# Performance work log

Measured on AMD Instinct MI355X. Metric: run time of the kernel, lower is better.

The kernel has to match this reference:

```python
import jax, jax.numpy as jnp
import numpy as np

N_A = 50000; N_B = 50000          # nodes per type
FD = 8; BINS = 32; EMB = 16       # discrete features, bins, per-feature embed dim
HID = 64; ZD = 32                 # hidden_dim, embed_dim
E = 800000                        # edges per relation (avg degree 16)


def setup_inputs() -> dict:
    key = jax.random.key(0)
    ks = iter(jax.random.split(key, 64))
    def nrm(shape, s=0.05):
        return jax.random.normal(next(ks), shape, jnp.float32) * s
    def ri(shape, hi):
        return jax.random.randint(next(ks), shape, 0, hi, dtype=jnp.int32)
    inp = {
        'x_A': ri((N_A, FD), BINS),
        'x_B': ri((N_B, FD), BINS),
        'ei_ab': ri((2, E), N_A),   # src in A, dst in B (N_A == N_B)
        'ei_ba': ri((2, E), N_B),
        'ei_aa': ri((2, E), N_A),
        # per-feature embedding tables [FD, BINS, EMB]
        'emb_A': nrm((FD, BINS, EMB)), 'emb_B': nrm((FD, BINS, EMB)),
        # pre_lin per node type (in = FD*EMB)
        'pre_W_A': nrm((FD * EMB, HID)), 'pre_b_A': nrm((HID,)),
        'pre_W_B': nrm((FD * EMB, HID)), 'pre_b_B': nrm((HID,)),
        # SAGEConv per relation: lin_l (on aggregated msgs, with bias), lin_r (root, no bias)
        'sage_l_W_ab': nrm((HID, HID)), 'sage_l_b_ab': nrm((HID,)), 'sage_r_W_ab': nrm((HID, HID)),
        'sage_l_W_ba': nrm((HID, HID)), 'sage_l_b_ba': nrm((HID,)), 'sage_r_W_ba': nrm((HID, HID)),
        'sage_l_W_aa': nrm((HID, HID)), 'sage_l_b_aa': nrm((HID,)), 'sage_r_W_aa': nrm((HID, HID)),
        # lin_proj per node type
        'proj_W_A': nrm((HID, ZD)), 'proj_b_A': nrm((ZD,)),
        'proj_W_B': nrm((HID, ZD)), 'proj_b_B': nrm((ZD,)),
        # feature heads per node type -> FD*BINS logits
        'head_W_A': nrm((ZD, FD * BINS)), 'head_b_A': nrm((FD * BINS,)),
        'head_W_B': nrm((ZD, FD * BINS)), 'head_b_B': nrm((FD * BINS,)),
        # bilinear edge decoders per relation: W [1, ZD, ZD], bias [1]
        'bil_W_ab': nrm((1, ZD, ZD)), 'bil_b_ab': nrm((1,)),
        'bil_W_ba': nrm((1, ZD, ZD)), 'bil_b_ba': nrm((1,)),
        'bil_W_aa': nrm((1, ZD, ZD)), 'bil_b_aa': nrm((1,)),
    }
    return inp


def _segment_mean(vals, idx, n):
    s = jax.ops.segment_sum(vals, idx, num_segments=n)
    c = jax.ops.segment_sum(jnp.ones((vals.shape[0], 1), vals.dtype), idx, num_segments=n)
    return s / jnp.maximum(c, 1.0)


def _sage(x_src, x_dst, ei, Wl, bl, Wr):
    # SAGEConv: lin_l(mean_{j in N(i)} x_j) + lin_r(x_i)
    m = _segment_mean(x_src[ei[0]], ei[1], x_dst.shape[0])
    return m @ Wl + bl + x_dst @ Wr


def _embed(x, emb):
    # emb: [FD, BINS, EMB]; x: [N, FD] ints -> [N, FD*EMB]
    e = emb[jnp.arange(FD)[None, :], x]            # [N, FD, EMB]
    return e.reshape(x.shape[0], FD * EMB)


def _bilinear(zs, zd, W, b):
    # nn.Bilinear: out_o = zs^T W_o zd + b_o ; here out dim 1, squeeze
    return (jnp.einsum('ei,oij,ej->eo', zs, W, zd) + b)[:, 0]


def _forward(x_A, x_B, ei_ab, ei_ba, ei_aa,
             emb_A, emb_B, pre_W_A, pre_b_A, pre_W_B, pre_b_B,
             sage_l_W_ab, sage_l_b_ab, sage_r_W_ab,
             sage_l_W_ba, sage_l_b_ba, sage_r_W_ba,
             sage_l_W_aa, sage_l_b_aa, sage_r_W_aa,
             proj_W_A, proj_b_A, proj_W_B, proj_b_B,
             head_W_A, head_b_A, head_W_B, head_b_B,
             bil_W_ab, bil_b_ab, bil_W_ba, bil_b_ba, bil_W_aa, bil_b_aa):
    # feature encoder + pre_lin + relu
    x0_A = jax.nn.relu(_embed(x_A, emb_A) @ pre_W_A + pre_b_A)
    x0_B = jax.nn.relu(_embed(x_B, emb_B) @ pre_W_B + pre_b_B)
    # HeteroConv(SAGEConv per relation, aggr='mean' over relations per dst type)
    h_B = _sage(x0_A, x0_B, ei_ab, sage_l_W_ab, sage_l_b_ab, sage_r_W_ab)
    h_A = (_sage(x0_B, x0_A, ei_ba, sage_l_W_ba, sage_l_b_ba, sage_r_W_ba)
           + _sage(x0_A, x0_A, ei_aa, sage_l_W_aa, sage_l_b_aa, sage_r_W_aa)) * 0.5
    # projection
    z_A = jax.nn.relu(h_A @ proj_W_A + proj_b_A)
    z_B = jax.nn.relu(h_B @ proj_W_B + proj_b_B)
    # feature decode
    fl_A = (z_A @ head_W_A + head_b_A).reshape(-1, FD, BINS)
    fl_B = (z_B @ head_W_B + head_b_B).reshape(-1, FD, BINS)
    # edge decode (bilinear on gathered endpoint embeddings)
    s_ab = _bilinear(z_A[ei_ab[0]], z_B[ei_ab[1]], bil_W_ab, bil_b_ab)
    s_ba = _bilinear(z_B[ei_ba[0]], z_A[ei_ba[1]], bil_W_ba, bil_b_ba)
    s_aa = _bilinear(z_A[ei_aa[0]], z_A[ei_aa[1]], bil_W_aa, bil_b_aa)
    return (z_A, z_B, fl_A, fl_B, s_ab, s_ba, s_aa)


def reference(x_A, x_B, ei_ab, ei_ba, ei_aa,
              emb_A, emb_B, pre_W_A, pre_b_A, pre_W_B, pre_b_B,
              sage_l_W_ab, sage_l_b_ab, sage_r_W_ab,
              sage_l_W_ba, sage_l_b_ba, sage_r_W_ba,
              sage_l_W_aa, sage_l_b_aa, sage_r_W_aa,
              proj_W_A, proj_b_A, proj_W_B, proj_b_B,
              head_W_A, head_b_A, head_W_B, head_b_B,
              bil_W_ab, bil_b_ab, bil_W_ba, bil_b_ba, bil_W_aa, bil_b_aa):
    return _forward(x_A, x_B, ei_ab, ei_ba, ei_aa,
                    emb_A, emb_B, pre_W_A, pre_b_A, pre_W_B, pre_b_B,
                    sage_l_W_ab, sage_l_b_ab, sage_r_W_ab,
                    sage_l_W_ba, sage_l_b_ba, sage_r_W_ba,
                    sage_l_W_aa, sage_l_b_aa, sage_r_W_aa,
                    proj_W_A, proj_b_A, proj_W_B, proj_b_B,
                    head_W_A, head_b_A, head_W_B, head_b_B,
                    bil_W_ab, bil_b_ab, bil_W_ba, bil_b_ba, bil_W_aa, bil_b_aa)
```

## Files before the change

kernel.cpp:

```cpp
#include <hip/hip_runtime.h>

typedef unsigned short u16;
typedef unsigned int u32;
typedef __attribute__((ext_vector_type(8))) short short8;
typedef __attribute__((ext_vector_type(4))) float f32x4;

constexpr int NA = 50000, NB = 50000;
constexpr int EMB = 16, HID = 64;
constexpr int NE = 800000;
constexpr int NBKT = 782;
constexpr int CAPB = 1536;
constexpr int EPB = 8192;
constexpr int BPR = (NE + EPB - 1) / EPB;

#define MFMA16(a, b, c) __builtin_amdgcn_mfma_f32_16x16x32_bf16(a, b, c, 0, 0, 0)

__device__ inline u16 f2bf(float f) {
  u32 b = __float_as_uint(f);
  return (u16)((b + 0x7FFFu + ((b >> 16) & 1u)) >> 16);
}
__device__ inline float bfl(u32 u) { return __uint_as_float(u << 16); }
__device__ inline float bfh(u32 u) { return __uint_as_float(u & 0xFFFF0000u); }
__device__ inline float bfs(u16 u) { return __uint_as_float((u32)u << 16); }

__global__ void __launch_bounds__(256) k_pre(
    const float* __restrict__ embA, const float* __restrict__ embB,
    const float* __restrict__ preWA, const float* __restrict__ preWB,
    float* __restrict__ T,
    const float* __restrict__ Wr_ba, const float* __restrict__ Wr_aa,
    const float* __restrict__ Wl_ba, const float* __restrict__ Wl_aa,
    const float* __restrict__ Wl_ab, const float* __restrict__ Wr_ab,
    const float* __restrict__ bl_ba, const float* __restrict__ bl_aa,
    const float* __restrict__ projWA, const float* __restrict__ projWB,
    const float* __restrict__ headWA, const float* __restrict__ headWB,
    const float* __restrict__ bilW_ba, const float* __restrict__ bilW_aa,
    const float* __restrict__ bilW_ab,
    u16* __restrict__ frag, float* __restrict__ bhA,
    const int* __restrict__ ei_ab, const int* __restrict__ ei_ba,
    const int* __restrict__ ei_aa, int* __restrict__ gcur,
    u32* __restrict__ buckets) {
  __shared__ int hist[NBKT];
  __shared__ int wcur[NBKT];
  int blk = blockIdx.x;
  int t = threadIdx.x;

  if (blk < 128) {
    int id = blk * 256 + t;
    int type = id >> 14;
    int rem = id & 16383;
    int col = rem >> 8;
    int fdbin = rem & 255;
    int fd = fdbin >> 5;
    const float* emb = type ? embB : embA;
    const float* W = type ? preWB : preWA;
    const float* e = emb + fdbin * EMB;
    const float* w = W + (fd * EMB) * HID + col;
    float s = 0.f;
#pragma unroll
    for (int j = 0; j < EMB; ++j) s += e[j] * w[j * HID];
    T[id] = s;
    return;
  }

  if (blk < 150) {
    int tid = (blk - 128) * 256 + t;
    if (tid >= 86 * 64) {
      int i = tid - 86 * 64;
      if (i < 64) bhA[i] = 0.5f * (bl_ba[i] + bl_aa[i]);
      return;
    }
    int f = tid >> 6, lane = tid & 63;
    int nidx = lane & 15, quad = lane >> 4;
    u16* dst = frag + (size_t)f * 512 + lane * 8;
#pragma unroll
    for (int j = 0; j < 8; ++j) {
      int kq = quad * 8 + j;
      float v;
      if (f < 24) {
        int s = f >> 2, nt = f & 3, k = s * 32 + kq, c = nt * 16 + nidx;
        v = (k < 64) ? 0.5f * (Wr_ba[k * 64 + c] + Wr_aa[k * 64 + c])
            : (k < 128) ? 0.5f * Wl_ba[(k - 64) * 64 + c]
                        : 0.5f * Wl_aa[(k - 128) * 64 + c];
      } else if (f < 28) {
        int g = f - 24, k = (g >> 1) * 32 + kq, c = (g & 1) * 16 + nidx;
        v = projWA[k * 32 + c];
      } else if (f < 44) {
        int c = (f - 28) * 16 + nidx;
        v = headWA[kq * 256 + c];
      } else if (f < 46) {
        int i2 = (f - 44) * 16 + nidx;
        v = bilW_ba[i2 * 32 + kq];
      } else if (f < 48) {
        int i2 = (f - 46) * 16 + nidx;
        v = bilW_aa[i2 * 32 + kq];
      } else if (f < 64) {
        int g = f - 48, s = g >> 2, nt = g & 3, k = s * 32 + kq, c = nt * 16 + nidx;
        v = (k < 64) ? Wr_ab[k * 64 + c] : Wl_ab[(k - 64) * 64 + c];
      } else if (f < 68) {
        int g = f - 64, k = (g >> 1) * 32 + kq, c = (g & 1) * 16 + nidx;
        v = projWB[k * 32 + c];
      } else if (f < 84) {
        int c = (f - 68) * 16 + nidx;
        v = headWB[kq * 256 + c];
      } else {
        int i2 = (f - 84) * 16 + nidx;
        v = bilW_ab[i2 * 32 + kq];
      }
      dst[j] = f2bf(v);
    }
    return;
  }

  int mblk = blk - 150;
  int rel = mblk / BPR;
  int lb = mblk - rel * BPR;
  const int* ei = rel == 0 ? ei_ab : (rel == 1 ? ei_ba : ei_aa);
  int e0 = lb * EPB;
  int n = min(EPB, NE - e0);
  for (int i = t; i < NBKT; i += 256) hist[i] = 0;
  __syncthreads();
  for (int i = t; i < n; i += 256) {
    int dstn = ei[NE + e0 + i];
    atomicAdd(&hist[dstn >> 6], 1);
  }
  __syncthreads();
  for (int i = t; i < NBKT; i += 256) {
    int c = hist[i];
    wcur[i] = (c > 0) ? atomicAdd(&gcur[rel * NBKT + i], c) : 0;
  }
  __syncthreads();
  for (int i = t; i < n; i += 256) {
    int src = ei[e0 + i];
    int dstn = ei[NE + e0 + i];
    int b = dstn >> 6;
    int pos = atomicAdd(&wcur[b], 1);
    if (pos < CAPB)
      buckets[(size_t)(rel * NBKT + b) * CAPB + pos] =
          ((u32)src << 6) | (u32)(dstn & 63);
  }
}

__global__ void __launch_bounds__(256) k_x0(const int* __restrict__ xA,
                                            const int* __restrict__ xB,
                                            const float* __restrict__ T,
                                            const float* __restrict__ biasA,
                                            const float* __restrict__ biasB,
                                            u16* __restrict__ x0A,
                                            u16* __restrict__ x0B) {
  extern __shared__ float Tl[];
  int blk = blockIdx.x;
  int type = blk >= 782;
  int lb = type ? blk - 782 : blk;
  const int* x = type ? xB : xA;
  const float* Tt = T + (type ? 16384 : 0);
  const float* bias = type ? biasB : biasA;
  u16* x0 = type ? x0B : x0A;
  const int N = NA;

  const float4* Tg = (const float4*)Tt;
  float4* Ts = (float4*)Tl;
  for (int i = threadIdx.x; i < 4096; i += 256) {
    int col = i >> 6, b4 = i & 63;
    Ts[col * 64 + ((b4 + 2 * (col >> 4)) & 63)] = Tg[i];
  }
  __syncthreads();
  int t = threadIdx.x;
  int r = t >> 2, q = t & 3;
  int row = lb * 64 + r;
  bool valid = row < N;
  int arow = valid ? row : (N - 1);
  const int4* xp = (const int4*)(x + arow * 8);
  int4 xa = xp[0], xb = xp[1];
  int bins[8] = {xa.x, xa.y, xa.z, xa.w, xb.x, xb.y, xb.z, xb.w};
  int c0 = q * 16;
  float acc[16];
#pragma unroll
  for (int j = 0; j < 16; ++j) acc[j] = bias[c0 + j];
#pragma unroll
  for (int fd = 0; fd < 8; ++fd) {
    int sb = ((fd * 32 + bins[fd]) + 8 * q) & 255;
#pragma unroll
    for (int j = 0; j < 16; ++j) acc[j] += Tl[(c0 + j) * 256 + sb];
  }
  if (valid) {
    u32 p[8];
#pragma unroll
    for (int j = 0; j < 8; ++j) {
      u16 lo = f2bf(fmaxf(acc[2 * j], 0.f));
      u16 hi = f2bf(fmaxf(acc[2 * j + 1], 0.f));
      p[j] = (u32)lo | ((u32)hi << 16);
    }
    u32* o = (u32*)(x0 + (size_t)row * 64 + c0);
    *(uint4*)o = *(uint4*)&p[0];
    *((uint4*)o + 1) = *(uint4*)&p[4];
  }
}

__global__ void __launch_bounds__(256) k_meansort_all(
    const u32* __restrict__ buckets, const int* __restrict__ cur,
    const u16* __restrict__ x0A, const u16* __restrict__ x0B,
    u16* __restrict__ mab, u16* __restrict__ mba, u16* __restrict__ maa) {
  __shared__ u32 ebuf[CAPB];
  __shared__ u16 csr[CAPB];
  __shared__ int dcnt[64], doff[64], wcur[64];
  int blk = blockIdx.x;
  int rel = blk / NBKT;
  int lb = blk - rel * NBKT;
  int t = threadIdx.x;
  const u16* x0 = (rel == 1) ? x0B : x0A;
  u16* out = rel == 0 ? mab : (rel == 1 ? mba : maa);
  int n = min(cur[blk], CAPB);
  const u32* bk = buckets + (size_t)blk * CAPB;
  if (t < 64) dcnt[t] = 0;
  __syncthreads();
  for (int i = t; i < n; i += 256) {
    u32 v = bk[i];
    ebuf[i] = v;
    atomicAdd(&dcnt[v & 63], 1);
  }
  __syncthreads();
  if (t == 0) {
    int s = 0;
#pragma unroll
    for (int d = 0; d < 64; ++d) {
      doff[d] = s;
      wcur[d] = s;
      s += dcnt[d];
    }
  }
  __syncthreads();
  for (int i = t; i < n; i += 256) {
    u32 v = ebuf[i];
    int p = atomicAdd(&wcur[v & 63], 1);
    csr[p] = (u16)(v >> 6);
  }
  __syncthreads();
  int lane = t & 63, w = t >> 6;
  int g = lane >> 4;
  int dim4 = (lane & 15) * 4;
  int base = lb * 64;
  for (int c = 0; c < 4; ++c) {
    int dloc = w * 16 + c * 4 + g;
    int dstn = base + dloc;
    if (dstn < 50000) {
      int off = doff[dloc], deg = dcnt[dloc];
      float a0 = 0.f, a1 = 0.f, a2 = 0.f, a3 = 0.f;
      int i = 0;
      for (; i + 4 <= deg; i += 4) {
        int s0 = csr[off + i], s1 = csr[off + i + 1];
        int s2 = csr[off + i + 2], s3 = csr[off + i + 3];
        uint2 v0 = *(const uint2*)(x0 + (size_t)s0 * 64 + dim4);
        uint2 v1 = *(const uint2*)(x0 + (size_t)s1 * 64 + dim4);
        uint2 v2 = *(const uint2*)(x0 + (size_t)s2 * 64 + dim4);
        uint2 v3 = *(const uint2*)(x0 + (size_t)s3 * 64 + dim4);
        a0 += bfl(v0.x) + bfl(v1.x) + bfl(v2.x) + bfl(v3.x);
        a1 += bfh(v0.x) + bfh(v1.x) + bfh(v2.x) + bfh(v3.x);
        a2 += bfl(v0.y) + bfl(v1.y) + bfl(v2.y) + bfl(v3.y);
        a3 += bfh(v0.y) + bfh(v1.y) + bfh(v2.y) + bfh(v3.y);
      }
      for (; i < deg; ++i) {
        int s0 = csr[off + i];
        uint2 v0 = *(const uint2*)(x0 + (size_t)s0 * 64 + dim4);
        a0 += bfl(v0.x);
        a1 += bfh(v0.x);
        a2 += bfl(v0.y);
        a3 += bfh(v0.y);
      }
      float inv = deg > 0 ? 1.f / (float)deg : 0.f;
      uint2 o;
      o.x = (u32)f2bf(a0 * inv) | ((u32)f2bf(a1 * inv) << 16);
      o.y = (u32)f2bf(a2 * inv) | ((u32)f2bf(a3 * inv) << 16);
      *(uint2*)(out + (size_t)dstn * 64 + dim4) = o;
    }
  }
}

template <int NS, int NY>
__device__ __forceinline__ void node_chain(
    const u16* __restrict__ x0, const u16* __restrict__ m1, const u16* __restrict__ m2,
    const u16* __restrict__ frag, int f1, int f2, int fy, int fh,
    const float* __restrict__ hbias, const float* __restrict__ projb,
    const float* __restrict__ headb,
    float* __restrict__ zout, float* __restrict__ flout,
    u16* __restrict__ zbf, u16* __restrict__ y1bf, u16* __restrict__ y2bf,
    int rows0, int N, u16* hld, u16* zld, int lane) {
  int nidx = lane & 15, quad = lane >> 4;
  size_t r0 = (size_t)min(rows0 + nidx, N - 1);
  size_t r1 = (size_t)min(rows0 + 16 + nidx, N - 1);

  f32x4 acc[2][4];
#pragma unroll
  for (int mt = 0; mt < 2; ++mt)
#pragma unroll
    for (int nt = 0; nt < 4; ++nt) acc[mt][nt] = {0.f, 0.f, 0.f, 0.f};
  const u16* mats[3] = {x0, m1, m2};
#pragma unroll
  for (int s = 0; s < NS; ++s) {
    const u16* src = mats[s >> 1];
    int koff = (s & 1) * 32 + quad * 8;
    short8 a0 = *(const short8*)(src + r0 * 64 + koff);
    short8 a1 = *(const short8*)(src + r1 * 64 + koff);
#pragma unroll
    for (int nt = 0; nt < 4; ++nt) {
      short8 b = *(const short8*)(frag + (size_t)(f1 + s * 4 + nt) * 512 + lane * 8);
      acc[0][nt] = MFMA16(a0, b, acc[0][nt]);
      acc[1][nt] = MFMA16(a1, b, acc[1][nt]);
    }
  }
#pragma unroll
  for (int mt = 0; mt < 2; ++mt)
#pragma unroll
    for (int nt = 0; nt < 4; ++nt) {
      int col = nt * 16 + nidx;
      float bb = hbias[col];
#pragma unroll
      for (int r2 = 0; r2 < 4; ++r2)
        hld[(mt * 16 + quad * 4 + r2) * 72 + col] = f2bf(acc[mt][nt][r2] + bb);
    }

  f32x4 zacc[2][2];
#pragma unroll
  for (int mt = 0; mt < 2; ++mt)
#pragma unroll
    for (int nt = 0; nt < 2; ++nt) zacc[mt][nt] = {0.f, 0.f, 0.f, 0.f};
#pragma unroll
  for (int s = 0; s < 2; ++s) {
    short8 a0 = *(const short8*)(hld + nidx * 72 + s * 32 + quad * 8);
    short8 a1 = *(const short8*)(hld + (16 + nidx) * 72 + s * 32 + quad * 8);
#pragma unroll
    for (int nt = 0; nt < 2; ++nt) {
      short8 b = *(const short8*)(frag + (size_t)(f2 + s * 2 + nt) * 512 + lane * 8);
      zacc[0][nt] = MFMA16(a0, b, zacc[0][nt]);
      zacc[1][nt] = MFMA16(a1, b, zacc[1][nt]);
    }
  }
#pragma unroll
  for (int mt = 0; mt < 2; ++mt)
#pragma unroll
    for (int nt = 0; nt < 2; ++nt) {
      int col = nt * 16 + nidx;
      float pb = projb[col];
#pragma unroll
      for (int r2 = 0; r2 < 4; ++r2) {
        int rl = mt * 16 + quad * 4 + r2;
        float zv = fmaxf(zacc[mt][nt][r2] + pb, 0.f);
        zld[rl * 40 + col] = f2bf(zv);
        int grow = rows0 + rl;
        if (grow < N) zout[(size_t)grow * 32 + col] = zv;
      }
    }
  {
    int rl = lane >> 1, hf = lane & 1;
    int grow = rows0 + rl;
    if (grow < N) {
      short8 v0 = *(const short8*)(zld + rl * 40 + hf * 16);
      short8 v1 = *(const short8*)(zld + rl * 40 + hf * 16 + 8);
      *(short8*)(zbf + (size_t)grow * 32 + hf * 16) = v0;
      *(short8*)(zbf + (size_t)grow * 32 + hf * 16 + 8) = v1;
    }
  }

  short8 az0 = *(const short8*)(zld + nidx * 40 + quad * 8);
  short8 az1 = *(const short8*)(zld + (16 + nidx) * 40 + quad * 8);
#pragma unroll
  for (int mat = 0; mat < NY; ++mat) {
    f32x4 ya[2][2];
#pragma unroll
    for (int mt = 0; mt < 2; ++mt)
#pragma unroll
      for (int nt = 0; nt < 2; ++nt) ya[mt][nt] = {0.f, 0.f, 0.f, 0.f};
#pragma unroll
    for (int nt = 0; nt < 2; ++nt) {
      short8 b = *(const short8*)(frag + (size_t)(fy + mat * 2 + nt) * 512 + lane * 8);
      ya[0][nt] = MFMA16(az0, b, ya[0][nt]);
      ya[1][nt] = MFMA16(az1, b, ya[1][nt]);
    }
#pragma unroll
    for (int mt = 0; mt < 2; ++mt)
#pragma unroll
      for (int nt = 0; nt < 2; ++nt)
#pragma unroll
        for (int r2 = 0; r2 < 4; ++r2)
          hld[(mt * 16 + quad * 4 + r2) * 40 + nt * 16 + nidx] = f2bf(ya[mt][nt][r2]);
    u16* yo = mat ? y2bf : y1bf;
    int rl = lane >> 1, hf = lane & 1;
    int grow = rows0 + rl;
    if (grow < N) {
      short8 v0 = *(const short8*)(hld + rl * 40 + hf * 16);
      short8 v1 = *(const short8*)(hld + rl * 40 + hf * 16 + 8);
      *(short8*)(yo + (size_t)grow * 32 + hf * 16) = v0;
      *(short8*)(yo + (size_t)grow * 32 + hf * 16 + 8) = v1;
    }
  }

  for (int chunk = 0; chunk < 4; ++chunk) {
    f32x4 fa[2][4];
#pragma unroll
    for (int mt = 0; mt < 2; ++mt)
#pragma unroll
      for (int nt = 0; nt < 4; ++nt) fa[mt][nt] = {0.f, 0.f, 0.f, 0.f};
#pragma unroll
    for (int nt = 0; nt < 4; ++nt) {
      short8 b = *(const short8*)(frag + (size_t)(fh + chunk * 4 + nt) * 512 + lane * 8);
      fa[0][nt] = MFMA16(az0, b, fa[0][nt]);
      fa[1][nt] = MFMA16(az1, b, fa[1][nt]);
    }
#pragma unroll
    for (int mt = 0; mt < 2; ++mt)
#pragma unroll
      for (int nt = 0; nt < 4; ++nt) {
        int col = chunk * 64 + nt * 16 + nidx;
        float hb = headb[col];
#pragma unroll
        for (int r2 = 0; r2 < 4; ++r2) {
          int grow = rows0 + mt * 16 + quad * 4 + r2;
          if (grow < N) flout[(size_t)grow * 256 + col] = fa[mt][nt][r2] + hb;
        }
      }
  }
}

__global__ void __launch_bounds__(256) k_node(
    const u16* __restrict__ x0A, const u16* __restrict__ mba, const u16* __restrict__ maa,
    const u16* __restrict__ x0B, const u16* __restrict__ mab,
    const u16* __restrict__ frag, const float* __restrict__ bhA,
    const float* __restrict__ bl_ab,
    const float* __restrict__ projbA, const float* __restrict__ headbA,
    const float* __restrict__ projbB, const float* __restrict__ headbB,
    float* __restrict__ zA, float* __restrict__ flA, u16* __restrict__ zAbf,
    u16* __restrict__ ybabf, u16* __restrict__ yaabf,
    float* __restrict__ zB, float* __restrict__ flB, u16* __restrict__ zBbf,
    u16* __restrict__ yabbf) {
  __shared__ u16 lds[4][3584];
  int t = threadIdx.x, lane = t & 63, w = t >> 6;
  u16* hld = &lds[w][0];
  u16* zld = &lds[w][2304];
  int blk = blockIdx.x;
  if (blk < 391) {
    node_chain<6, 2>(x0A, mba, maa, frag, 0, 24, 44, 28, bhA, projbA, headbA,
                     zA, flA, zAbf, ybabf, yaabf, blk * 128 + w * 32, NA, hld, zld, lane);
  } else {
    node_chain<4, 1>(x0B, mab, mab, frag, 48, 64, 84, 68, bl_ab, projbB, headbB,
                     zB, flB, zBbf, yabbf, yabbf, (blk - 391) * 128 + w * 32, NB, hld,
                     zld, lane);
  }
}

__global__ void k_bil_all(const int* __restrict__ ei_ab, const int* __restrict__ ei_ba,
                          const int* __restrict__ ei_aa,
                          const u16* __restrict__ zA, const u16* __restrict__ zB,
                          const u16* __restrict__ yab, const u16* __restrict__ yba,
                          const u16* __restrict__ yaa,
                          const float* __restrict__ b_ab, const float* __restrict__ b_ba,
                          const float* __restrict__ b_aa,
                          float* __restrict__ s_ab, float* __restrict__ s_ba,
                          float* __restrict__ s_aa) {
  int e = blockIdx.x * 256 + threadIdx.x;
  int rel = e / NE;
  int le = e - rel * NE;
  const int* ei = rel == 0 ? ei_ab : (rel == 1 ? ei_ba : ei_aa);
  const u16* zs = (rel == 1) ? zB : zA;
  const u16* yd = rel == 0 ? yab : (rel == 1 ? yba : yaa);
  const float* bb = rel == 0 ? b_ab : (rel == 1 ? b_ba : b_aa);
  float* so = rel == 0 ? s_ab : (rel == 1 ? s_ba : s_aa);
  int si = ei[le], di = ei[NE + le];
  const uint4* zp = (const uint4*)(zs + (size_t)si * 32);
  const uint4* yp = (const uint4*)(yd + (size_t)di * 32);
  float acc = 0.f;
#pragma unroll
  for (int i = 0; i < 4; ++i) {
    uint4 a = zp[i], c = yp[i];
    acc += bfl(a.x) * bfl(c.x) + bfh(a.x) * bfh(c.x);
    acc += bfl(a.y) * bfl(c.y) + bfh(a.y) * bfh(c.y);
    acc += bfl(a.z) * bfl(c.z) + bfh(a.z) * bfh(c.z);
    acc += bfl(a.w) * bfl(c.w) + bfh(a.w) * bfh(c.w);
  }
  so[le] = acc + bb[0];
}

extern "C" void kernel_launch(void* const* d_in, const int* in_sizes, int n_in,
                              void* d_out, int out_size, void* d_ws, size_t ws_size,
                              hipStream_t stream) {
  const int* xA = (const int*)d_in[0];
  const int* xB = (const int*)d_in[1];
  const int* ei_ab = (const int*)d_in[2];
  const int* ei_ba = (const int*)d_in[3];
  const int* ei_aa = (const int*)d_in[4];
  const float* embA = (const float*)d_in[5];
  const float* embB = (const float*)d_in[6];
  const float* preWA = (const float*)d_in[7];
  const float* prebA = (const float*)d_in[8];
  const float* preWB = (const float*)d_in[9];
  const float* prebB = (const float*)d_in[10];
  const float* Wl_ab = (const float*)d_in[11];
  const float* bl_ab = (const float*)d_in[12];
  const float* Wr_ab = (const float*)d_in[13];
  const float* Wl_ba = (const float*)d_in[14];
  const float* bl_ba = (const float*)d_in[15];
  const float* Wr_ba = (const float*)d_in[16];
  const float* Wl_aa = (const float*)d_in[17];
  const float* bl_aa = (const float*)d_in[18];
  const float* Wr_aa = (const float*)d_in[19];
  const float* projWA = (const float*)d_in[20];
  const float* projbA = (const float*)d_in[21];
  const float* projWB = (const float*)d_in[22];
  const float* projbB = (const float*)d_in[23];
  const float* headWA = (const float*)d_in[24];
  const float* headbA = (const float*)d_in[25];
  const float* headWB = (const float*)d_in[26];
  const float* headbB = (const float*)d_in[27];
  const float* bilW_ab = (const float*)d_in[28];
  const float* bilb_ab = (const float*)d_in[29];
  const float* bilW_ba = (const float*)d_in[30];
  const float* bilb_ba = (const float*)d_in[31];
  const float* bilW_aa = (const float*)d_in[32];
  const float* bilb_aa = (const float*)d_in[33];

  float* out = (float*)d_out;
  float* zA = out;
  float* zB = out + 1600000;
  float* flA = out + 3200000;
  float* flB = out + 16000000;
  float* s_ab = out + 28800000;
  float* s_ba = out + 29600000;
  float* s_aa = out + 30400000;

  char* ws = (char*)d_ws;
  float* T = (float*)(ws + 0);
  u16* x0Abf = (u16*)(ws + 131072);
  u16* x0Bbf = (u16*)(ws + 6531072);
  u16* mabbf = (u16*)(ws + 12931072);
  u16* mbabf = (u16*)(ws + 19331072);
  u16* maabf = (u16*)(ws + 25731072);
  u16* zAbf = (u16*)(ws + 32131072);
  u16* zBbf = (u16*)(ws + 35331072);
  u16* yabbf = (u16*)(ws + 38531072);
  u16* ybabf = (u16*)(ws + 41731072);
  u16* yaabf = (u16*)(ws + 44931072);
  int* cur = (int*)(ws + 48131072);
  u16* frag = (u16*)(ws + 48731072);
  float* bhA = (float*)(ws + 48819136);

  u32* buckets = (u32*)flA;

  hipMemsetAsync(cur, 0, 3 * NBKT * sizeof(int), stream);
  k_pre<<<150 + 3 * BPR, 256, 0, stream>>>(
      embA, embB, preWA, preWB, T,
      Wr_ba, Wr_aa, Wl_ba, Wl_aa, Wl_ab, Wr_ab, bl_ba, bl_aa,
      projWA, projWB, headWA, headWB, bilW_ba, bilW_aa, bilW_ab,
      frag, bhA, ei_ab, ei_ba, ei_aa, cur, buckets);
  k_x0<<<2 * 782, 256, 65536, stream>>>(xA, xB, T, prebA, prebB, x0Abf, x0Bbf);
  k_meansort_all<<<3 * NBKT, 256, 0, stream>>>(buckets, cur, x0Abf, x0Bbf,
                                               mabbf, mbabf, maabf);
  k_node<<<782, 256, 0, stream>>>(x0Abf, mbabf, maabf, x0Bbf, mabbf, frag, bhA,
                                  bl_ab, projbA, headbA, projbB, headbB,
                                  zA, flA, zAbf, ybabf, yaabf, zB, flB, zBbf, yabbf);
  k_bil_all<<<3 * NE / 256, 256, 0, stream>>>(ei_ab, ei_ba, ei_aa, zAbf, zBbf,
                                              yabbf, ybabf, yaabf,
                                              bilb_ab, bilb_ba, bilb_aa,
                                              s_ab, s_ba, s_aa);
}
```

Baseline: 397.9 us.

## Shrink bucket-sort chunks, reorder pre blocks, unroll gather, pair edges in bilinear

Edge bucketing uses smaller chunks (2048 edges per block), giving more blocks, and those blocks are scheduled first in the pre kernel ahead of the table and fragment work. The mean-aggregation gather gains an 8-way unrolled loop so more loads are in flight. The bilinear edge scorer now handles two edges per thread with vectorised index loads and float2 stores. Together these aim to raise parallelism and memory-level parallelism. The cost is more global atomics on the bucket cursors and higher register pressure.

```diff
diff --git a/kernel.cpp b/kernel.cpp
--- a/kernel.cpp
+++ b/kernel.cpp
@@ -10,8 +10,9 @@
 constexpr int NE = 800000;
 constexpr int NBKT = 782;
 constexpr int CAPB = 1536;
-constexpr int EPB = 8192;
+constexpr int EPB = 2048;
 constexpr int BPR = (NE + EPB - 1) / EPB;
+constexpr int MSB = 3 * BPR;
 
 #define MFMA16(a, b, c) __builtin_amdgcn_mfma_f32_16x16x32_bf16(a, b, c, 0, 0, 0)
 
@@ -44,8 +45,38 @@
   int blk = blockIdx.x;
   int t = threadIdx.x;
 
-  if (blk < 128) {
-    int id = blk * 256 + t;
+  if (blk < MSB) {
+    int rel = blk / BPR;
+    int lb = blk - rel * BPR;
+    const int* ei = rel == 0 ? ei_ab : (rel == 1 ? ei_ba : ei_aa);
+    int e0 = lb * EPB;
+    int n = min(EPB, NE - e0);
+    for (int i = t; i < NBKT; i += 256) hist[i] = 0;
+    __syncthreads();
+    for (int i = t; i < n; i += 256) {
+      int dstn = ei[NE + e0 + i];
+      atomicAdd(&hist[dstn >> 6], 1);
+    }
+    __syncthreads();
+    for (int i = t; i < NBKT; i += 256) {
+      int c = hist[i];
+      wcur[i] = (c > 0) ? atomicAdd(&gcur[rel * NBKT + i], c) : 0;
+    }
+    __syncthreads();
+    for (int i = t; i < n; i += 256) {
+      int src = ei[e0 + i];
+      int dstn = ei[NE + e0 + i];
+      int b = dstn >> 6;
+      int pos = atomicAdd(&wcur[b], 1);
+      if (pos < CAPB)
+        buckets[(size_t)(rel * NBKT + b) * CAPB + pos] =
+            ((u32)src << 6) | (u32)(dstn & 63);
+    }
+    return;
+  }
+
+  if (blk < MSB + 128) {
+    int id = (blk - MSB) * 256 + t;
     int type = id >> 14;
     int rem = id & 16383;
     int col = rem >> 8;
@@ -62,81 +93,50 @@
     return;
   }
 
-  if (blk < 150) {
-    int tid = (blk - 128) * 256 + t;
-    if (tid >= 86 * 64) {
-      int i = tid - 86 * 64;
-      if (i < 64) bhA[i] = 0.5f * (bl_ba[i] + bl_aa[i]);
-      return;
-    }
-    int f = tid >> 6, lane = tid & 63;
-    int nidx = lane & 15, quad = lane >> 4;
-    u16* dst = frag + (size_t)f * 512 + lane * 8;
-#pragma unroll
-    for (int j = 0; j < 8; ++j) {
-      int kq = quad * 8 + j;
-      float v;
-      if (f < 24) {
-        int s = f >> 2, nt = f & 3, k = s * 32 + kq, c = nt * 16 + nidx;
-        v = (k < 64) ? 0.5f * (Wr_ba[k * 64 + c] + Wr_aa[k * 64 + c])
-            : (k < 128) ? 0.5f * Wl_ba[(k - 64) * 64 + c]
-                        : 0.5f * Wl_aa[(k - 128) * 64 + c];
-      } else if (f < 28) {
-        int g = f - 24, k = (g >> 1) * 32 + kq, c = (g & 1) * 16 + nidx;
-        v = projWA[k * 32 + c];
-      } else if (f < 44) {
-        int c = (f - 28) * 16 + nidx;
-        v = headWA[kq * 256 + c];
-      } else if (f < 46) {
-        int i2 = (f - 44) * 16 + nidx;
-        v = bilW_ba[i2 * 32 + kq];
-      } else if (f < 48) {
-        int i2 = (f - 46) * 16 + nidx;
-        v = bilW_aa[i2 * 32 + kq];
-      } else if (f < 64) {
-        int g = f - 48, s = g >> 2, nt = g & 3, k = s * 32 + kq, c = nt * 16 + nidx;
-        v = (k < 64) ? Wr_ab[k * 64 + c] : Wl_ab[(k - 64) * 64 + c];
-      } else if (f < 68) {
-        int g = f - 64, k = (g >> 1) * 32 + kq, c = (g & 1) * 16 + nidx;
-        v = projWB[k * 32 + c];
-      } else if (f < 84) {
-        int c = (f - 68) * 16 + nidx;
-        v = headWB[kq * 256 + c];
-      } else {
-        int i2 = (f - 84) * 16 + nidx;
-        v = bilW_ab[i2 * 32 + kq];
-      }
-      dst[j] = f2bf(v);
-    }
+  int tid = (blk - MSB - 128) * 256 + t;
+  if (tid >= 86 * 64) {
+    int i = tid - 86 * 64;
+    if (i < 64) bhA[i] = 0.5f * (bl_ba[i] + bl_aa[i]);
     return;
   }
-
-  int mblk = blk - 150;
-  int rel = mblk / BPR;
-  int lb = mblk - rel * BPR;
-  const int* ei = rel == 0 ? ei_ab : (rel == 1 ? ei_ba : ei_aa);
-  int e0 = lb * EPB;
-  int n = min(EPB, NE - e0);
-  for (int i = t; i < NBKT; i += 256) hist[i] = 0;
-  __syncthreads();
-  for (int i = t; i < n; i += 256) {
-    int dstn = ei[NE + e0 + i];
-    atomicAdd(&hist[dstn >> 6], 1);
-  }
-  __syncthreads();
-  for (int i = t; i < NBKT; i += 256) {
-    int c = hist[i];
-    wcur[i] = (c > 0) ? atomicAdd(&gcur[rel * NBKT + i], c) : 0;
-  }
-  __syncthreads();
-  for (int i = t; i < n; i += 256) {
-    int src = ei[e0 + i];
-    int dstn = ei[NE + e0 + i];
-    int b = dstn >> 6;
-    int pos = atomicAdd(&wcur[b], 1);
-    if (pos < CAPB)
-      buckets[(size_t)(rel * NBKT + b) * CAPB + pos] =
-          ((u32)src << 6) | (u32)(dstn & 63);
+  int f = tid >> 6, lane = tid & 63;
+  int nidx = lane & 15, quad = lane >> 4;
+  u16* dst = frag + (size_t)f * 512 + lane * 8;
+#pragma unroll
+  for (int j = 0; j < 8; ++j) {
+    int kq = quad * 8 + j;
+    float v;
+    if (f < 24) {
+      int s = f >> 2, nt = f & 3, k = s * 32 + kq, c = nt * 16 + nidx;
+      v = (k < 64) ? 0.5f * (Wr_ba[k * 64 + c] + Wr_aa[k * 64 + c])
+          : (k < 128) ? 0.5f * Wl_ba[(k - 64) * 64 + c]
+                      : 0.5f * Wl_aa[(k - 128) * 64 + c];
+    } else if (f < 28) {
+      int g = f - 24, k = (g >> 1) * 32 + kq, c = (g & 1) * 16 + nidx;
+      v = projWA[k * 32 + c];
+    } else if (f < 44) {
+      int c = (f - 28) * 16 + nidx;
+      v = headWA[kq * 256 + c];
+    } else if (f < 46) {
+      int i2 = (f - 44) * 16 + nidx;
+      v = bilW_ba[i2 * 32 + kq];
+    } else if (f < 48) {
+      int i2 = (f - 46) * 16 + nidx;
+      v = bilW_aa[i2 * 32 + kq];
+    } else if (f < 64) {
+      int g = f - 48, s = g >> 2, nt = g & 3, k = s * 32 + kq, c = nt * 16 + nidx;
+      v = (k < 64) ? Wr_ab[k * 64 + c] : Wl_ab[(k - 64) * 64 + c];
+    } else if (f < 68) {
+      int g = f - 64, k = (g >> 1) * 32 + kq, c = (g & 1) * 16 + nidx;
+      v = projWB[k * 32 + c];
+    } else if (f < 84) {
+      int c = (f - 68) * 16 + nidx;
+      v = headWB[kq * 256 + c];
+    } else {
+      int i2 = (f - 84) * 16 + nidx;
+      v = bilW_ab[i2 * 32 + kq];
+    }
+    dst[j] = f2bf(v);
   }
 }
 
@@ -246,21 +246,36 @@
       int off = doff[dloc], deg = dcnt[dloc];
       float a0 = 0.f, a1 = 0.f, a2 = 0.f, a3 = 0.f;
       int i = 0;
+      for (; i + 8 <= deg; i += 8) {
+        uint2 v0 = *(const uint2*)(x0 + (size_t)csr[off + i] * 64 + dim4);
+        uint2 v1 = *(const uint2*)(x0 + (size_t)csr[off + i + 1] * 64 + dim4);
+        uint2 v2 = *(const uint2*)(x0 + (size_t)csr[off + i + 2] * 64 + dim4);
+        uint2 v3 = *(const uint2*)(x0 + (size_t)csr[off + i + 3] * 64 + dim4);
+        uint2 v4 = *(const uint2*)(x0 + (size_t)csr[off + i + 4] * 64 + dim4);
+        uint2 v5 = *(const uint2*)(x0 + (size_t)csr[off + i + 5] * 64 + dim4);
+        uint2 v6 = *(const uint2*)(x0 + (size_t)csr[off + i + 6] * 64 + dim4);
+        uint2 v7 = *(const uint2*)(x0 + (size_t)csr[off + i + 7] * 64 + dim4);
+        a0 += bfl(v0.x) + bfl(v1.x) + bfl(v2.x) + bfl(v3.x) +
+              bfl(v4.x) + bfl(v5.x) + bfl(v6.x) + bfl(v7.x);
+        a1 += bfh(v0.x) + bfh(v1.x) + bfh(v2.x) + bfh(v3.x) +
+              bfh(v4.x) + bfh(v5.x) + bfh(v6.x) + bfh(v7.x);
+        a2 += bfl(v0.y) + bfl(v1.y) + bfl(v2.y) + bfl(v3.y) +
+              bfl(v4.y) + bfl(v5.y) + bfl(v6.y) + bfl(v7.y);
+        a3 += bfh(v0.y) + bfh(v1.y) + bfh(v2.y) + bfh(v3.y) +
+              bfh(v4.y) + bfh(v5.y) + bfh(v6.y) + bfh(v7.y);
+      }
       for (; i + 4 <= deg; i += 4) {
-        int s0 = csr[off + i], s1 = csr[off + i + 1];
-        int s2 = csr[off + i + 2], s3 = csr[off + i + 3];
-        uint2 v0 = *(const uint2*)(x0 + (size_t)s0 * 64 + dim4);
-        uint2 v1 = *(const uint2*)(x0 + (size_t)s1 * 64 + dim4);
-        uint2 v2 = *(const uint2*)(x0 + (size_t)s2 * 64 + dim4);
-        uint2 v3 = *(const uint2*)(x0 + (size_t)s3 * 64 + dim4);
+        uint2 v0 = *(const uint2*)(x0 + (size_t)csr[off + i] * 64 + dim4);
+        uint2 v1 = *(const uint2*)(x0 + (size_t)csr[off + i + 1] * 64 + dim4);
+        uint2 v2 = *(const uint2*)(x0 + (size_t)csr[off + i + 2] * 64 + dim4);
+        uint2 v3 = *(const uint2*)(x0 + (size_t)csr[off + i + 3] * 64 + dim4);
         a0 += bfl(v0.x) + bfl(v1.x) + bfl(v2.x) + bfl(v3.x);
         a1 += bfh(v0.x) + bfh(v1.x) + bfh(v2.x) + bfh(v3.x);
         a2 += bfl(v0.y) + bfl(v1.y) + bfl(v2.y) + bfl(v3.y);
         a3 += bfh(v0.y) + bfh(v1.y) + bfh(v2.y) + bfh(v3.y);
       }
       for (; i < deg; ++i) {
-        int s0 = csr[off + i];
-        uint2 v0 = *(const uint2*)(x0 + (size_t)s0 * 64 + dim4);
+        uint2 v0 = *(const uint2*)(x0 + (size_t)csr[off + i] * 64 + dim4);
         a0 += bfl(v0.x);
         a1 += bfh(v0.x);
         a2 += bfl(v0.y);
@@ -446,36 +461,51 @@
   }
 }
 
-__global__ void k_bil_all(const int* __restrict__ ei_ab, const int* __restrict__ ei_ba,
-                          const int* __restrict__ ei_aa,
-                          const u16* __restrict__ zA, const u16* __restrict__ zB,
-                          const u16* __restrict__ yab, const u16* __restrict__ yba,
-                          const u16* __restrict__ yaa,
-                          const float* __restrict__ b_ab, const float* __restrict__ b_ba,
-                          const float* __restrict__ b_aa,
-                          float* __restrict__ s_ab, float* __restrict__ s_ba,
-                          float* __restrict__ s_aa) {
-  int e = blockIdx.x * 256 + threadIdx.x;
-  int rel = e / NE;
-  int le = e - rel * NE;
+__global__ void __launch_bounds__(256) k_bil_all(
+    const int* __restrict__ ei_ab, const int* __restrict__ ei_ba,
+    const int* __restrict__ ei_aa,
+    const u16* __restrict__ zA, const u16* __restrict__ zB,
+    const u16* __restrict__ yab, const u16* __restrict__ yba,
+    const u16* __restrict__ yaa,
+    const float* __restrict__ b_ab, const float* __restrict__ b_ba,
+    const float* __restrict__ b_aa,
+    float* __restrict__ s_ab, float* __restrict__ s_ba,
+    float* __restrict__ s_aa) {
+  constexpr int NEH = NE / 2;
+  int p = blockIdx.x * 256 + threadIdx.x;
+  if (p >= 3 * NEH) return;
+  int rel = p / NEH;
+  int lp = p - rel * NEH;
+  int le = 2 * lp;
   const int* ei = rel == 0 ? ei_ab : (rel == 1 ? ei_ba : ei_aa);
   const u16* zs = (rel == 1) ? zB : zA;
   const u16* yd = rel == 0 ? yab : (rel == 1 ? yba : yaa);
   const float* bb = rel == 0 ? b_ab : (rel == 1 ? b_ba : b_aa);
   float* so = rel == 0 ? s_ab : (rel == 1 ? s_ba : s_aa);
-  int si = ei[le], di = ei[NE + le];
-  const uint4* zp = (const uint4*)(zs + (size_t)si * 32);
-  const uint4* yp = (const uint4*)(yd + (size_t)di * 32);
-  float acc = 0.f;
+  int2 si = *(const int2*)(ei + le);
+  int2 di = *(const int2*)(ei + NE + le);
+  const uint4* zp0 = (const uint4*)(zs + (size_t)si.x * 32);
+  const uint4* yp0 = (const uint4*)(yd + (size_t)di.x * 32);
+  const uint4* zp1 = (const uint4*)(zs + (size_t)si.y * 32);
+  const uint4* yp1 = (const uint4*)(yd + (size_t)di.y * 32);
+  float acc0 = 0.f, acc1 = 0.f;
 #pragma unroll
   for (int i = 0; i < 4; ++i) {
-    uint4 a = zp[i], c = yp[i];
-    acc += bfl(a.x) * bfl(c.x) + bfh(a.x) * bfh(c.x);
-    acc += bfl(a.y) * bfl(c.y) + bfh(a.y) * bfh(c.y);
-    acc += bfl(a.z) * bfl(c.z) + bfh(a.z) * bfh(c.z);
-    acc += bfl(a.w) * bfl(c.w) + bfh(a.w) * bfh(c.w);
-  }
-  so[le] = acc + bb[0];
+    uint4 a0 = zp0[i], c0 = yp0[i];
+    uint4 a1 = zp1[i], c1 = yp1[i];
+    acc0 += bfl(a0.x) * bfl(c0.x) + bfh(a0.x) * bfh(c0.x);
+    acc0 += bfl(a0.y) * bfl(c0.y) + bfh(a0.y) * bfh(c0.y);
+    acc0 += bfl(a0.z) * bfl(c0.z) + bfh(a0.z) * bfh(c0.z);
+    acc0 += bfl(a0.w) * bfl(c0.w) + bfh(a0.w) * bfh(c0.w);
+    acc1 += bfl(a1.x) * bfl(c1.x) + bfh(a1.x) * bfh(c1.x);
+    acc1 += bfl(a1.y) * bfl(c1.y) + bfh(a1.y) * bfh(c1.y);
+    acc1 += bfl(a1.z) * bfl(c1.z) + bfh(a1.z) * bfh(c1.z);
+    acc1 += bfl(a1.w) * bfl(c1.w) + bfh(a1.w) * bfh(c1.w);
+  }
+  float2 o;
+  o.x = acc0 + bb[0];
+  o.y = acc1 + bb[0];
+  *(float2*)(so + le) = o;
 }
 
 extern "C" void kernel_launch(void* const* d_in, const int* in_sizes, int n_in,
@@ -544,7 +574,7 @@
   u32* buckets = (u32*)flA;
 
   hipMemsetAsync(cur, 0, 3 * NBKT * sizeof(int), stream);
-  k_pre<<<150 + 3 * BPR, 256, 0, stream>>>(
+  k_pre<<<MSB + 150, 256, 0, stream>>>(
       embA, embB, preWA, preWB, T,
       Wr_ba, Wr_aa, Wl_ba, Wl_aa, Wl_ab, Wr_ab, bl_ba, bl_aa,
       projWA, projWB, headWA, headWB, bilW_ba, bilW_aa, bilW_ab,
@@ -555,8 +585,7 @@
   k_node<<<782, 256, 0, stream>>>(x0Abf, mbabf, maabf, x0Bbf, mabbf, frag, bhA,
                                   bl_ab, projbA, headbA, projbB, headbB,
                                   zA, flA, zAbf, ybabf, yaabf, zB, flB, zBbf, yabbf);
-  k_bil_all<<<3 * NE / 256, 256, 0, stream>>>(ei_ab, ei_ba, ei_aa, zAbf, zBbf,
-                                              yabbf, ybabf, yaabf,
-                                              bilb_ab, bilb_ba, bilb_aa,
-                                              s_ab, s_ba, s_aa);
-}
+  k_bil_all<<<(3 * (NE / 2) + 255) / 256, 256, 0, stream>>>(
+      ei_ab, ei_ba, ei_aa, zAbf, zBbf, yabbf, ybabf, yaabf,
+      bilb_ab, bilb_ba, bilb_aa, s_ab, s_ba, s_aa);
+}
```

New measurement: 435.2 us. +9.4%, slower.
